# Kernel tuning notes

Measured on AMD Instinct MI355X. Metric: run time of the kernel, lower is better.

Reference implementation:

```python
import jax, jax.numpy as jnp
import numpy as np

B, N, HID = 4, 16384, 512
H, M = 8, 32          # num_heads, num_slices
D = HID // H          # head_dim = 64


def setup_inputs() -> dict:
    key = jax.random.key(0)
    ks = jax.random.split(key, 8)
    std = 0.02
    return {
        "x": jax.random.normal(ks[0], (B, N, HID), jnp.float32),
        # Linear weights stored as [in, out] (y = x @ W + b)
        "wkv_w": jax.random.normal(ks[1], (HID, 2 * HID), jnp.float32) * std,
        "wkv_b": jnp.zeros((2 * HID,), jnp.float32),
        "wtq": jax.random.normal(ks[2], (H, M, D), jnp.float32) * std,
        "alpha": jnp.ones((H,), jnp.float32),
        "qkv_w": jax.random.normal(ks[3], (HID, 3 * HID), jnp.float32) * std,
        "out_w": jax.random.normal(ks[4], (HID, HID), jnp.float32) * std,
        "out_b": jnp.zeros((HID,), jnp.float32),
    }


def _split_heads(t):  # [b, n, h*d] -> [b, h, n, d]
    b, n, _ = t.shape
    return t.reshape(b, n, H, D).transpose(0, 2, 1, 3)


def _mha(q, k, v):
    scale = q.shape[-1] ** -0.5
    dots = jnp.einsum('bhqd,bhkd->bhqk', q, k) * scale
    attn = jax.nn.softmax(dots, axis=-1)
    out = jnp.einsum('bhqk,bhkd->bhqd', attn, v)
    return out, attn


def reference(x, wkv_w, wkv_b, wtq, alpha, qkv_w, out_w, out_b):
    kv = x @ wkv_w + wkv_b                      # [b, n, 2*hid]
    xk, xv = kv[..., :HID], kv[..., HID:]
    xk = _split_heads(xk)                       # [b, h, n, d]
    xv = _split_heads(xv)

    # slot/slice cross-attention: softmax over the slice axis m (axis=-2)
    slice_scores = jnp.einsum('hmd,bhnd->bhmn', wtq, xk)
    slice_weights = jax.nn.softmax(slice_scores * alpha[None, :, None, None], axis=-2)
    slice_token = jnp.einsum('bhmn,bhnd->bhmd', slice_weights, xv)
    slice_token = slice_token / (slice_weights.sum(axis=-1, keepdims=True) + 1e-5)
    slice_token = slice_token.transpose(0, 2, 1, 3).reshape(B, M, HID)  # b m (h d)

    # small inner MHA over the m=32 slices
    qkv = slice_token @ qkv_w                   # [b, m, 3*hid]
    q_t = _split_heads(qkv[..., :HID])
    k_t = _split_heads(qkv[..., HID:2 * HID])
    v_t = _split_heads(qkv[..., 2 * HID:])
    out_token, attn_weights = _mha(q_t, k_t, v_t)

    # scatter slice outputs back to n positions
    out = jnp.einsum('bhmd,bhmn->bhnd', out_token, slice_weights)
    out = out.transpose(0, 2, 1, 3).reshape(B, N, HID)  # b n (h d)
    out = out @ out_w + out_b
    return out, slice_weights, alpha, jnp.zeros((H, M), jnp.float32), attn_weights
```

## Files before the change

### kernel.cpp

```cpp
#include <hip/hip_runtime.h>

#define B_ 4
#define N_ 16384
#define HID_ 512
#define H_ 8
#define M_ 32
#define D_ 64

typedef __attribute__((ext_vector_type(8))) short short8;
typedef __attribute__((ext_vector_type(4))) float f32x4;

__device__ __forceinline__ short f2bf(float f) {
    unsigned u = __float_as_uint(f);
    u += 0x7fffu + ((u >> 16) & 1u);
    return (short)(u >> 16);
}
__device__ __forceinline__ float bf2f(short s) {
    return __uint_as_float(((unsigned)(unsigned short)s) << 16);
}
__device__ __forceinline__ unsigned pack2(float a, float b) {
    return (unsigned)(unsigned short)f2bf(a) | ((unsigned)(unsigned short)f2bf(b) << 16);
}
__device__ __forceinline__ void gl_lds16(const short* g, short* l) {
    __builtin_amdgcn_global_load_lds((const __attribute__((address_space(1))) unsigned*)g,
                                     (__attribute__((address_space(3))) unsigned*)l, 16, 0, 0);
}

__global__ void k_misc(const float* __restrict__ alpha, float* __restrict__ a_out,
                       float* __restrict__ z_out, const float* __restrict__ wtq,
                       short* __restrict__ wtq_bf) {
    int i = blockIdx.x * 256 + threadIdx.x;
    wtq_bf[i] = f2bf(wtq[i]);
    if (blockIdx.x == 0) {
        int t = threadIdx.x;
        if (t < H_) a_out[t] = alpha[t];
        z_out[t] = 0.f;
    }
}

__global__ void k_cvt(const float* __restrict__ src, short* __restrict__ dst) {
    int i = blockIdx.x * 256 + threadIdx.x;
    const f32x4* s = (const f32x4*)(src) + (size_t)i * 2;
    f32x4 a = s[0], b = s[1];
    short8 o;
    o[0] = f2bf(a[0]); o[1] = f2bf(a[1]); o[2] = f2bf(a[2]); o[3] = f2bf(a[3]);
    o[4] = f2bf(b[0]); o[5] = f2bf(b[1]); o[6] = f2bf(b[2]); o[7] = f2bf(b[3]);
    ((short8*)dst)[i] = o;
}

__global__ void k_wt(const float* __restrict__ w, short* __restrict__ wt) {
    int e = blockIdx.x * 256 + threadIdx.x;
    int nn = e >> 9, kk = e & 511;
    wt[e] = f2bf(w[kk * 1024 + nn]);
}

template <bool OUT_BF16>
__global__ __launch_bounds__(256, 2)
void mfma_gemm(const short* __restrict__ A, const short* __restrict__ Bt,
               const float* __restrict__ bias, void* __restrict__ Cv,
               int K, int Ncols, int b_stride, int rows_per_b) {
    __shared__ short As[128 * 32];
    __shared__ short Bs[128 * 32];
    const int t = threadIdx.x;
    const int col0 = blockIdx.x * 128;
    const int row0 = blockIdx.y * 128;
    const short* Bblk = Bt;
    if (b_stride) Bblk += (size_t)(row0 / rows_per_b) * (size_t)b_stride;

    const int r_a = t >> 2;
    const int c_a = (t & 3) << 3;
    const short* Ap = A + (size_t)(row0 + r_a) * K + c_a;
    const short* Bp = Bblk + (size_t)(col0 + r_a) * K + c_a;
    short* As0 = &As[t << 3];
    short* Bs0 = &Bs[t << 3];
    const size_t rowskip = (size_t)64 * K;

    const int w = t >> 6;
    const int L = t & 63;
    const int wm = (w >> 1) << 6;
    const int wn = (w & 1) << 6;
    const int lm = L & 15;
    const int lq = L >> 4;

    f32x4 acc[4][4];
#pragma unroll
    for (int i = 0; i < 4; ++i)
#pragma unroll
        for (int j = 0; j < 4; ++j) acc[i][j] = (f32x4){0.f, 0.f, 0.f, 0.f};

    for (int k0 = 0; k0 < K; k0 += 32) {
        gl_lds16(Ap + k0, As0);
        gl_lds16(Ap + k0 + rowskip, As0 + 2048);
        gl_lds16(Bp + k0, Bs0);
        gl_lds16(Bp + k0 + rowskip, Bs0 + 2048);
        __syncthreads();
        short8 af[4], bfr[4];
#pragma unroll
        for (int i = 0; i < 4; ++i)
            af[i] = *(const short8*)&As[((wm + (i << 4) + lm) << 5) + (lq << 3)];
#pragma unroll
        for (int j = 0; j < 4; ++j)
            bfr[j] = *(const short8*)&Bs[((wn + (j << 4) + lm) << 5) + (lq << 3)];
#pragma unroll
        for (int i = 0; i < 4; ++i)
#pragma unroll
            for (int j = 0; j < 4; ++j)
                acc[i][j] = __builtin_amdgcn_mfma_f32_16x16x32_bf16(af[i], bfr[j], acc[i][j], 0, 0, 0);
        __syncthreads();
    }
#pragma unroll
    for (int i = 0; i < 4; ++i) {
#pragma unroll
        for (int j = 0; j < 4; ++j) {
            const int gr = row0 + wm + (i << 4) + (lq << 2);
            const int gc = col0 + wn + (j << 4) + lm;
            const float bv = bias[gc];
#pragma unroll
            for (int r = 0; r < 4; ++r) {
                float v = acc[i][j][r] + bv;
                if constexpr (OUT_BF16)
                    ((short*)Cv)[(size_t)(gr + r) * Ncols + gc] = f2bf(v);
                else
                    ((float*)Cv)[(size_t)(gr + r) * Ncols + gc] = v;
            }
        }
    }
}

__global__ __attribute__((amdgpu_flat_work_group_size(256, 256), amdgpu_waves_per_eu(3, 3)))
void k_slice2(const short* __restrict__ kv, const short* __restrict__ wtq_bf,
              const float* __restrict__ alpha, float* __restrict__ sw_out,
              short* __restrict__ swT, float* __restrict__ pnum, float* __restrict__ pws) {
    __shared__ __attribute__((aligned(16))) short wT_s[M_ * 256];
    __shared__ __attribute__((aligned(16))) short xvT_s[D_ * 256];
    const int t = threadIdx.x;
    const int bx = blockIdx.x;
    const int chunk = bx & 63;
    const int h = (bx >> 6) & 7;
    const int b = bx >> 9;
    const int w = t >> 6;
    const int L = t & 63;
    const int lm = L & 15;
    const int g = L >> 4;
    const int n0 = chunk * 256;
    const size_t rowb = (size_t)(b * N_ + n0);
    const float al = alpha[h];

    short8 xv8[8];
    const short8* xvp = (const short8*)(kv + (rowb + t) * 1024 + HID_ + h * 64);
#pragma unroll
    for (int i = 0; i < 8; ++i) xv8[i] = xvp[i];

    short8 bq[2][2];
    const short* wq = wtq_bf + h * (M_ * D_);
#pragma unroll
    for (int mt = 0; mt < 2; ++mt)
#pragma unroll
        for (int ks = 0; ks < 2; ++ks)
            bq[mt][ks] = *(const short8*)(wq + (mt * 16 + lm) * 64 + ks * 32 + g * 8);

    f32x4 s[4][2];
#pragma unroll
    for (int nt = 0; nt < 4; ++nt)
#pragma unroll
        for (int mt = 0; mt < 2; ++mt) s[nt][mt] = (f32x4){0.f, 0.f, 0.f, 0.f};
#pragma unroll
    for (int ks = 0; ks < 2; ++ks) {
        short8 aq[4];
#pragma unroll
        for (int nt = 0; nt < 4; ++nt)
            aq[nt] = *(const short8*)(kv + (rowb + w * 64 + nt * 16 + lm) * 1024 +
                                      h * 64 + ks * 32 + g * 8);
#pragma unroll
        for (int nt = 0; nt < 4; ++nt)
#pragma unroll
            for (int mt = 0; mt < 2; ++mt)
                s[nt][mt] = __builtin_amdgcn_mfma_f32_16x16x32_bf16(aq[nt], bq[mt][ks], s[nt][mt], 0, 0, 0);
    }

#pragma unroll
    for (int nt = 0; nt < 4; ++nt)
#pragma unroll
        for (int r = 0; r < 4; ++r) {
            float v0 = s[nt][0][r] * al, v1 = s[nt][1][r] * al;
            float mx = fmaxf(v0, v1);
#pragma unroll
            for (int d2 = 1; d2 < 16; d2 <<= 1) mx = fmaxf(mx, __shfl_xor(mx, d2));
            float e0 = __expf(v0 - mx), e1 = __expf(v1 - mx);
            float sm = e0 + e1;
#pragma unroll
            for (int d2 = 1; d2 < 16; d2 <<= 1) sm += __shfl_xor(sm, d2);
            float inv = 1.f / sm;
            s[nt][0][r] = e0 * inv;
            s[nt][1][r] = e1 * inv;
        }

    float ws0 = 0.f, ws1 = 0.f;
#pragma unroll
    for (int nt = 0; nt < 4; ++nt) {
        const int nn = w * 64 + nt * 16 + g * 4;
#pragma unroll
        for (int mt = 0; mt < 2; ++mt) {
            const int m = mt * 16 + lm;
            *(f32x4*)(sw_out + ((size_t)((b * 8 + h) * 32 + m)) * N_ + n0 + nn) = s[nt][mt];
            float w4 = s[nt][mt][0] + s[nt][mt][1] + s[nt][mt][2] + s[nt][mt][3];
            if (mt == 0) ws0 += w4; else ws1 += w4;
            unsigned lo = pack2(s[nt][mt][0], s[nt][mt][1]);
            unsigned hi = pack2(s[nt][mt][2], s[nt][mt][3]);
            *(uint2*)(wT_s + m * 256 + (nn ^ ((m & 7) << 3))) = make_uint2(lo, hi);
        }
    }

#pragma unroll
    for (int i = 0; i < 8; ++i)
#pragma unroll
        for (int j = 0; j < 8; ++j)
            xvT_s[(i * 8 + j) * 256 + (t ^ (j << 3))] = xv8[i][j];

    __syncthreads();

    const int dcol = w * 16 + lm;
    f32x4 acc2[2];
    acc2[0] = (f32x4){0.f, 0.f, 0.f, 0.f};
    acc2[1] = (f32x4){0.f, 0.f, 0.f, 0.f};
#pragma unroll
    for (int ks = 0; ks < 8; ++ks) {
        const int kb = ks * 32 + g * 8;
        short8 bv = *(const short8*)(xvT_s + dcol * 256 + (kb ^ ((lm & 7) << 3)));
#pragma unroll
        for (int mt = 0; mt < 2; ++mt) {
            const int m = mt * 16 + lm;
            short8 av = *(const short8*)(wT_s + m * 256 + (kb ^ ((lm & 7) << 3)));
            acc2[mt] = __builtin_amdgcn_mfma_f32_16x16x32_bf16(av, bv, acc2[mt], 0, 0, 0);
        }
    }

    {
        unsigned pk[16];
#pragma unroll
        for (int mp = 0; mp < 16; ++mp) {
            unsigned a0 = (unsigned short)wT_s[(2 * mp) * 256 + (t ^ (((2 * mp) & 7) << 3))];
            unsigned a1 = (unsigned short)wT_s[(2 * mp + 1) * 256 + (t ^ (((2 * mp + 1) & 7) << 3))];
            pk[mp] = a0 | (a1 << 16);
        }
        short8* swtp = (short8*)(swT + (rowb + t) * 256 + h * 32);
#pragma unroll
        for (int q = 0; q < 4; ++q) {
            short8 v;
            v[0] = (short)(pk[4 * q] & 0xffff);     v[1] = (short)(pk[4 * q] >> 16);
            v[2] = (short)(pk[4 * q + 1] & 0xffff); v[3] = (short)(pk[4 * q + 1] >> 16);
            v[4] = (short)(pk[4 * q + 2] & 0xffff); v[5] = (short)(pk[4 * q + 2] >> 16);
            v[6] = (short)(pk[4 * q + 3] & 0xffff); v[7] = (short)(pk[4 * q + 3] >> 16);
            swtp[q] = v;
        }
    }

    float* pn = pnum + ((size_t)((b * 8 + h) * 64 + chunk)) * 2048;
#pragma unroll
    for (int mt = 0; mt < 2; ++mt)
#pragma unroll
        for (int r = 0; r < 4; ++r)
            pn[(mt * 16 + g * 4 + r) * 64 + dcol] = acc2[mt][r];

    ws0 += __shfl_xor(ws0, 16); ws0 += __shfl_xor(ws0, 32);
    ws1 += __shfl_xor(ws1, 16); ws1 += __shfl_xor(ws1, 32);
    if (L < 16) {
        float* pw = pws + (((size_t)((b * 8 + h) * 64 + chunk)) * 4 + w) * 32;
        pw[lm] = ws0;
        pw[16 + lm] = ws1;
    }
}

__global__ __launch_bounds__(256)
void k_reduce(const float* __restrict__ pnum, const float* __restrict__ pws,
              float* __restrict__ num, float* __restrict__ wsum) {
    const int bid = blockIdx.x, t = threadIdx.x;
    if (bid < 256) {
        int e = bid * 256 + t;
        int bh = e >> 11, md = e & 2047;
        const float* p = pnum + (size_t)bh * 64 * 2048 + md;
        float s = 0.f;
#pragma unroll 4
        for (int c = 0; c < 64; ++c) s += p[c * 2048];
        num[e] = s;
    } else {
        int e = (bid - 256) * 256 + t;
        int bh = e >> 5, m = e & 31;
        const float* p = pws + (size_t)bh * 64 * 4 * 32 + m;
        float s = 0.f;
#pragma unroll 4
        for (int cw = 0; cw < 256; ++cw) s += p[cw * 32];
        wsum[e] = s;
    }
}

__global__ __launch_bounds__(256, 2)
void k_qkv(const float* __restrict__ num, const float* __restrict__ wsum,
           const float* __restrict__ qkv_w, float* __restrict__ qkv) {
    __shared__ float st_s[512 * 32];
    const int t = threadIdx.x;
    const int b = blockIdx.y;
    for (int p = 0; p < 64; ++p) {
        int idx = p * 256 + t;
        int m = idx & 31, k = idx >> 5;
        int h = k >> 6, d = k & 63;
        float wsv = wsum[(b * H_ + h) * M_ + m];
        st_s[k * 32 + m] = num[((size_t)(b * H_ + h) * M_ + m) * 64 + d] / (wsv + 1e-5f);
    }
    __syncthreads();
    const int m = t >> 3;
    const int c0 = blockIdx.x * 64 + (t & 7) * 8;
    float acc[8] = {};
    for (int k = 0; k < 512; ++k) {
        float sv = st_s[k * 32 + m];
        const f32x4* wp = (const f32x4*)(qkv_w + (size_t)k * 1536 + c0);
        f32x4 w0 = wp[0], w1 = wp[1];
        acc[0] += sv * w0[0]; acc[1] += sv * w0[1]; acc[2] += sv * w0[2]; acc[3] += sv * w0[3];
        acc[4] += sv * w1[0]; acc[5] += sv * w1[1]; acc[6] += sv * w1[2]; acc[7] += sv * w1[3];
    }
    float* dst = qkv + (size_t)(b * M_ + m) * 1536 + c0;
#pragma unroll
    for (int i = 0; i < 8; ++i) dst[i] = acc[i];
}

__global__ __launch_bounds__(256)
void k_mha(const float* __restrict__ qkv, float* __restrict__ attn_out,
           float* __restrict__ ot) {
    __shared__ float q_s[32 * 65], k_s[32 * 65], v_s[32 * 65];
    __shared__ float s_s[32 * 33], p_s[32 * 33];
    const int bx = blockIdx.x;
    const int b = bx >> 3, h = bx & 7;
    const int t = threadIdx.x;
    for (int p = 0; p < 8; ++p) {
        int idx = p * 256 + t;
        int m = idx >> 6, d = idx & 63;
        size_t base = (size_t)(b * M_ + m) * 1536 + h * 64 + d;
        q_s[m * 65 + d] = qkv[base];
        k_s[m * 65 + d] = qkv[base + 512];
        v_s[m * 65 + d] = qkv[base + 1024];
    }
    __syncthreads();
    for (int p = 0; p < 4; ++p) {
        int c = p * 256 + t;
        int m = c >> 5, mm = c & 31;
        float a = 0.f;
#pragma unroll
        for (int d = 0; d < 64; ++d) a += q_s[m * 65 + d] * k_s[mm * 65 + d];
        s_s[m * 33 + mm] = a * 0.125f;
    }
    __syncthreads();
    if (t < 32) {
        float mx = -1e30f;
        for (int mm = 0; mm < 32; ++mm) mx = fmaxf(mx, s_s[t * 33 + mm]);
        float sum = 0.f;
        for (int mm = 0; mm < 32; ++mm) {
            float e = __expf(s_s[t * 33 + mm] - mx);
            p_s[t * 33 + mm] = e;
            sum += e;
        }
        float inv = 1.f / sum;
        for (int mm = 0; mm < 32; ++mm) {
            float av = p_s[t * 33 + mm] * inv;
            p_s[t * 33 + mm] = av;
            attn_out[((size_t)(b * H_ + h) * M_ + t) * M_ + mm] = av;
        }
    }
    __syncthreads();
    const int m = t >> 3, d0 = (t & 7) * 8;
    float acc[8] = {};
    for (int mm = 0; mm < 32; ++mm) {
        float av = p_s[m * 33 + mm];
#pragma unroll
        for (int j = 0; j < 8; ++j) acc[j] += av * v_s[mm * 65 + d0 + j];
    }
    float* dst = ot + ((size_t)(b * H_ + h) * M_ + m) * 64 + d0;
#pragma unroll
    for (int j = 0; j < 8; ++j) dst[j] = acc[j];
}

__global__ __launch_bounds__(256)
void k_p(const float* __restrict__ ot, const float* __restrict__ out_w,
         short* __restrict__ Pt) {
    __shared__ float ot_s[32 * 65];
    const int bh = blockIdx.y;
    const int b = bh >> 3, h = bh & 7;
    const int t = threadIdx.x;
    for (int p = 0; p < 8; ++p) {
        int idx = p * 256 + t;
        int m = idx >> 6, d = idx & 63;
        ot_s[m * 65 + d] = ot[(size_t)bh * (M_ * 64) + idx];
    }
    __syncthreads();
    const int j = blockIdx.x * 128 + (t & 127);
    const int mh = (t >> 7) * 16;
    float acc[16] = {};
    for (int d = 0; d < 64; ++d) {
        float ow = out_w[(size_t)(h * 64 + d) * HID_ + j];
#pragma unroll
        for (int i = 0; i < 16; ++i) acc[i] += ot_s[(mh + i) * 65 + d] * ow;
    }
    short* dst = Pt + ((size_t)b * HID_ + j) * (H_ * M_) + h * M_ + mh;
#pragma unroll
    for (int i = 0; i < 16; i += 2) *(unsigned*)(dst + i) = pack2(acc[i], acc[i + 1]);
}

extern "C" void kernel_launch(void* const* d_in, const int* in_sizes, int n_in,
                              void* d_out, int out_size, void* d_ws, size_t ws_size,
                              hipStream_t stream) {
    const float* x     = (const float*)d_in[0];
    const float* wkv_w = (const float*)d_in[1];
    const float* wkv_b = (const float*)d_in[2];
    const float* wtq   = (const float*)d_in[3];
    const float* alpha = (const float*)d_in[4];
    const float* qkv_w = (const float*)d_in[5];
    const float* out_w = (const float*)d_in[6];
    const float* out_b = (const float*)d_in[7];

    float* out       = (float*)d_out;
    float* sw_out    = out + (size_t)B_ * N_ * HID_;
    float* alpha_out = sw_out + (size_t)B_ * H_ * M_ * N_;
    float* zeros_out = alpha_out + H_;
    float* attn_out  = zeros_out + H_ * M_;

    short* x_bf = (short*)sw_out;
    float* pnum = out;
    float* pws  = out + 4194304;

    char* ws = (char*)d_ws;
    short* kv   = (short*)(ws);
    short* swT  = (short*)(ws + 134217728);
    short* wkvT = (short*)(ws + 167772160);
    short* Pt   = (short*)(ws + 168820736);
    float* num  = (float*)(ws + 169869312);
    float* wsum = (float*)(ws + 170131456);
    float* qkvb = (float*)(ws + 170135552);
    float* ot   = (float*)(ws + 170921984);
    short* wtq_bf = (short*)(ws + 170921984);

    k_misc<<<64, 256, 0, stream>>>(alpha, alpha_out, zeros_out, wtq, wtq_bf);
    k_cvt<<<16384, 256, 0, stream>>>(x, x_bf);
    k_wt<<<2048, 256, 0, stream>>>(wkv_w, wkvT);
    mfma_gemm<true><<<dim3(8, 512), 256, 0, stream>>>(
        x_bf, wkvT, wkv_b, (void*)kv, 512, 1024, 0, 1 << 30);
    k_slice2<<<2048, 256, 0, stream>>>(kv, wtq_bf, alpha, sw_out, swT, pnum, pws);
    k_reduce<<<260, 256, 0, stream>>>(pnum, pws, num, wsum);
    k_qkv<<<dim3(24, 4), 256, 0, stream>>>(num, wsum, qkv_w, qkvb);
    k_mha<<<32, 256, 0, stream>>>(qkvb, attn_out, ot);
    k_p<<<dim3(4, 32), 256, 0, stream>>>(ot, out_w, Pt);
    mfma_gemm<false><<<dim3(4, 512), 256, 0, stream>>>(
        swT, Pt, out_b, (void*)out, 256, 512, 131072, 16384);
}
```

Before: 597.1 us.

## Split slice kernel into score and weighted-sum passes; remap GEMM blocks; tile weight transpose

The fused slice kernel becomes two kernels. k_score computes the softmax slice weights at higher occupancy and writes them out. k_wsum reads those weights back from global memory, converts them to bf16 into LDS and runs the weighted-V MFMA. The GEMM block index is remapped so consecutive workgroup IDs are spread in strides of eight, likely to spread tiles across XCDs for L2 locality, and the weight transpose now goes through an LDS tile for coalesced access. The split adds an extra global round trip of the fp32 slice weights (about 67MB read) and one more kernel launch, in exchange for lower register pressure and better occupancy.

```diff
diff --git a/kernel.cpp b/kernel.cpp
--- a/kernel.cpp
+++ b/kernel.cpp
@@ -48,22 +48,39 @@
     ((short8*)dst)[i] = o;
 }
 
-__global__ void k_wt(const float* __restrict__ w, short* __restrict__ wt) {
-    int e = blockIdx.x * 256 + threadIdx.x;
-    int nn = e >> 9, kk = e & 511;
-    wt[e] = f2bf(w[kk * 1024 + nn]);
+__global__ __launch_bounds__(256)
+void k_wt(const float* __restrict__ w, short* __restrict__ wt) {
+    __shared__ float ls[64][65];
+    const int t = threadIdx.x;
+    const int n0 = blockIdx.x * 64, k0 = blockIdx.y * 64;
+#pragma unroll
+    for (int p = 0; p < 16; ++p) {
+        int idx = p * 256 + t;
+        int kk = idx >> 6, nn = idx & 63;
+        ls[kk][nn] = w[(size_t)(k0 + kk) * 1024 + n0 + nn];
+    }
+    __syncthreads();
+#pragma unroll
+    for (int p = 0; p < 16; ++p) {
+        int idx = p * 256 + t;
+        int nn = idx >> 6, kk = idx & 63;
+        wt[(size_t)(n0 + nn) * 512 + k0 + kk] = f2bf(ls[kk][nn]);
+    }
 }
 
 template <bool OUT_BF16>
 __global__ __launch_bounds__(256, 2)
 void mfma_gemm(const short* __restrict__ A, const short* __restrict__ Bt,
                const float* __restrict__ bias, void* __restrict__ Cv,
-               int K, int Ncols, int b_stride, int rows_per_b) {
+               int K, int Ncols, int b_stride, int rows_per_b, int lgx) {
     __shared__ short As[128 * 32];
     __shared__ short Bs[128 * 32];
     const int t = threadIdx.x;
-    const int col0 = blockIdx.x * 128;
-    const int row0 = blockIdx.y * 128;
+    const int nwg = gridDim.x * gridDim.y;
+    int id = blockIdx.y * gridDim.x + blockIdx.x;
+    id = (id & 7) * (nwg >> 3) + (id >> 3);
+    const int col0 = (id & ((1 << lgx) - 1)) * 128;
+    const int row0 = (id >> lgx) * 128;
     const short* Bblk = Bt;
     if (b_stride) Bblk += (size_t)(row0 / rows_per_b) * (size_t)b_stride;
 
@@ -127,12 +144,10 @@
     }
 }
 
-__global__ __attribute__((amdgpu_flat_work_group_size(256, 256), amdgpu_waves_per_eu(3, 3)))
-void k_slice2(const short* __restrict__ kv, const short* __restrict__ wtq_bf,
-              const float* __restrict__ alpha, float* __restrict__ sw_out,
-              short* __restrict__ swT, float* __restrict__ pnum, float* __restrict__ pws) {
-    __shared__ __attribute__((aligned(16))) short wT_s[M_ * 256];
-    __shared__ __attribute__((aligned(16))) short xvT_s[D_ * 256];
+__global__ __launch_bounds__(256, 4)
+void k_score(const short* __restrict__ kv, const short* __restrict__ wtq_bf,
+             const float* __restrict__ alpha, float* __restrict__ sw_out,
+             float* __restrict__ pws) {
     const int t = threadIdx.x;
     const int bx = blockIdx.x;
     const int chunk = bx & 63;
@@ -146,11 +161,6 @@
     const size_t rowb = (size_t)(b * N_ + n0);
     const float al = alpha[h];
 
-    short8 xv8[8];
-    const short8* xvp = (const short8*)(kv + (rowb + t) * 1024 + HID_ + h * 64);
-#pragma unroll
-    for (int i = 0; i < 8; ++i) xv8[i] = xvp[i];
-
     short8 bq[2][2];
     const short* wq = wtq_bf + h * (M_ * D_);
 #pragma unroll
@@ -205,9 +215,52 @@
             *(f32x4*)(sw_out + ((size_t)((b * 8 + h) * 32 + m)) * N_ + n0 + nn) = s[nt][mt];
             float w4 = s[nt][mt][0] + s[nt][mt][1] + s[nt][mt][2] + s[nt][mt][3];
             if (mt == 0) ws0 += w4; else ws1 += w4;
-            unsigned lo = pack2(s[nt][mt][0], s[nt][mt][1]);
-            unsigned hi = pack2(s[nt][mt][2], s[nt][mt][3]);
-            *(uint2*)(wT_s + m * 256 + (nn ^ ((m & 7) << 3))) = make_uint2(lo, hi);
+        }
+    }
+    ws0 += __shfl_xor(ws0, 16); ws0 += __shfl_xor(ws0, 32);
+    ws1 += __shfl_xor(ws1, 16); ws1 += __shfl_xor(ws1, 32);
+    if (L < 16) {
+        float* pw = pws + (((size_t)((b * 8 + h) * 64 + chunk)) * 4 + w) * 32;
+        pw[lm] = ws0;
+        pw[16 + lm] = ws1;
+    }
+}
+
+__global__ __attribute__((amdgpu_flat_work_group_size(256, 256), amdgpu_waves_per_eu(3, 3)))
+void k_wsum(const short* __restrict__ kv, const float* __restrict__ sw_out,
+            short* __restrict__ swT, float* __restrict__ pnum) {
+    __shared__ __attribute__((aligned(16))) short wT_s[M_ * 256];
+    __shared__ __attribute__((aligned(16))) short xvT_s[D_ * 256];
+    const int t = threadIdx.x;
+    const int bx = blockIdx.x;
+    const int chunk = bx & 63;
+    const int h = (bx >> 6) & 7;
+    const int b = bx >> 9;
+    const int w = t >> 6;
+    const int L = t & 63;
+    const int lm = L & 15;
+    const int g = L >> 4;
+    const int n0 = chunk * 256;
+    const size_t rowb = (size_t)(b * N_ + n0);
+
+    short8 xv8[8];
+    const short8* xvp = (const short8*)(kv + (rowb + t) * 1024 + HID_ + h * 64);
+#pragma unroll
+    for (int i = 0; i < 8; ++i) xv8[i] = xvp[i];
+
+    {
+        const int m = t >> 3, i = t & 7;
+        const int xr = (m & 7) << 3;
+        const float* rp = sw_out + ((size_t)((b * 8 + h) * 32 + m)) * N_ + n0 + i * 32;
+#pragma unroll
+        for (int q = 0; q < 4; ++q) {
+            f32x4 a = ((const f32x4*)rp)[2 * q];
+            f32x4 c = ((const f32x4*)rp)[2 * q + 1];
+            int nn = i * 32 + q * 8;
+            short8 v;
+            v[0] = f2bf(a[0]); v[1] = f2bf(a[1]); v[2] = f2bf(a[2]); v[3] = f2bf(a[3]);
+            v[4] = f2bf(c[0]); v[5] = f2bf(c[1]); v[6] = f2bf(c[2]); v[7] = f2bf(c[3]);
+            *(short8*)(wT_s + m * 256 + (nn ^ xr)) = v;
         }
     }
 
@@ -261,14 +314,6 @@
 #pragma unroll
         for (int r = 0; r < 4; ++r)
             pn[(mt * 16 + g * 4 + r) * 64 + dcol] = acc2[mt][r];
-
-    ws0 += __shfl_xor(ws0, 16); ws0 += __shfl_xor(ws0, 32);
-    ws1 += __shfl_xor(ws1, 16); ws1 += __shfl_xor(ws1, 32);
-    if (L < 16) {
-        float* pw = pws + (((size_t)((b * 8 + h) * 64 + chunk)) * 4 + w) * 32;
-        pw[lm] = ws0;
-        pw[16 + lm] = ws1;
-    }
 }
 
 __global__ __launch_bounds__(256)
@@ -439,14 +484,15 @@
 
     k_misc<<<64, 256, 0, stream>>>(alpha, alpha_out, zeros_out, wtq, wtq_bf);
     k_cvt<<<16384, 256, 0, stream>>>(x, x_bf);
-    k_wt<<<2048, 256, 0, stream>>>(wkv_w, wkvT);
+    k_wt<<<dim3(16, 8), 256, 0, stream>>>(wkv_w, wkvT);
     mfma_gemm<true><<<dim3(8, 512), 256, 0, stream>>>(
-        x_bf, wkvT, wkv_b, (void*)kv, 512, 1024, 0, 1 << 30);
-    k_slice2<<<2048, 256, 0, stream>>>(kv, wtq_bf, alpha, sw_out, swT, pnum, pws);
+        x_bf, wkvT, wkv_b, (void*)kv, 512, 1024, 0, 1 << 30, 3);
+    k_score<<<2048, 256, 0, stream>>>(kv, wtq_bf, alpha, sw_out, pws);
+    k_wsum<<<2048, 256, 0, stream>>>(kv, sw_out, swT, pnum);
     k_reduce<<<260, 256, 0, stream>>>(pnum, pws, num, wsum);
     k_qkv<<<dim3(24, 4), 256, 0, stream>>>(num, wsum, qkv_w, qkvb);
     k_mha<<<32, 256, 0, stream>>>(qkvb, attn_out, ot);
     k_p<<<dim3(4, 32), 256, 0, stream>>>(ot, out_w, Pt);
     mfma_gemm<false><<<dim3(4, 512), 256, 0, stream>>>(
-        swT, Pt, out_b, (void*)out, 256, 512, 131072, 16384);
-}
+        swT, Pt, out_b, (void*)out, 256, 512, 131072, 16384, 2);
+}
```

After: 571.5 us. -4.3%, faster.
